# Optimization experiments

Hardware: AMD Instinct MI355X
Metric: run time of the kernel (lower is better)

Reference implementation:

```python
import jax, jax.numpy as jnp
import numpy as np

SELF_LOOP_EPS = 0.5

def setup_inputs() -> dict:
    key = jax.random.key(0)
    k1, k2 = jax.random.split(key)
    spatial_nodes = jax.random.normal(k1, (16, 2048, 64), dtype=jnp.float32)
    temporal_nodes = jax.random.normal(k2, (16, 64, 64), dtype=jnp.float32)
    return {"spatial_nodes": spatial_nodes, "temporal_nodes": temporal_nodes}

def reference(spatial_nodes, temporal_nodes):
    # concat spatial and temporal node embeddings along the node axis: [B, N+T, D]
    node_embs = jnp.concatenate([spatial_nodes, temporal_nodes], axis=1)
    # batched gram matrix: [B, M, M], M = N+T
    adj = jnp.einsum('bnf,bmf->bnm', node_embs, node_embs)
    adj = jnp.tanh(jax.nn.relu(adj))
    M = adj.shape[1]
    # add scaled self loops
    adj = adj + jnp.eye(M, dtype=adj.dtype) * SELF_LOOP_EPS
    # the torch module additionally extracts per-batch nonzero (edge_index, edge_weight)
    # lists; that is data-dependent stream compaction. The dense adj (plus its nonzero
    # mask) carries the identical information in a jit-compatible fixed-shape form.
    return adj
```

## Files before the change

### kernel.cpp

```cpp
#include <hip/hip_runtime.h>
#include <hip/hip_fp16.h>


#define B_BATCH   16
#define N_SPATIAL 2048
#define T_TEMP    64
#define M_NODES   2112
#define D_FEAT    64
#define TILE      64
#define LDSK      72
#define CSTR      68

#define TILES_PER_BATCH 1089
#define TOTAL_TILES     17424
#define TILES_PER_XCD   2178

typedef _Float16 f16x8 __attribute__((ext_vector_type(8)));
typedef float    f32x4 __attribute__((ext_vector_type(4)));

__global__ __launch_bounds__(256, 4)
void gram_tanh_mfma(const float* __restrict__ sp,
                    const float* __restrict__ tp,
                    float* __restrict__ out)
{
    const int lin = blockIdx.x;
    const int t   = (lin & 7) * TILES_PER_XCD + (lin >> 3);
    const int b   = t / TILES_PER_BATCH;
    const int r   = t - b * TILES_PER_BATCH;
    const int ti  = r / 33;
    const int tj  = r - ti * 33;

    __shared__ __align__(16) _Float16 As[TILE][LDSK];
    __shared__ __align__(16) _Float16 Bs[TILE][LDSK];
    __shared__ __align__(16) float    Ct[TILE][CSTR];

    const int tid = threadIdx.x;

    {
        const int row = tid >> 2;
        const int kb  = (tid & 3) * 16;
        const float* srcA = (ti < 32)
            ? sp + ((size_t)b * N_SPATIAL + (size_t)ti * TILE) * D_FEAT
            : tp + (size_t)b * T_TEMP * D_FEAT;
        const float* srcB = (tj < 32)
            ? sp + ((size_t)b * N_SPATIAL + (size_t)tj * TILE) * D_FEAT
            : tp + (size_t)b * T_TEMP * D_FEAT;
        const float4* pa = (const float4*)(srcA + (size_t)row * D_FEAT + kb);
        const float4* pb = (const float4*)(srcB + (size_t)row * D_FEAT + kb);

        f16x8 ha0, ha1, hb0, hb1;
        #pragma unroll
        for (int u = 0; u < 2; ++u) {
            float4 a = pa[u];
            ha0[u*4+0] = (_Float16)a.x; ha0[u*4+1] = (_Float16)a.y;
            ha0[u*4+2] = (_Float16)a.z; ha0[u*4+3] = (_Float16)a.w;
            float4 bb = pb[u];
            hb0[u*4+0] = (_Float16)bb.x; hb0[u*4+1] = (_Float16)bb.y;
            hb0[u*4+2] = (_Float16)bb.z; hb0[u*4+3] = (_Float16)bb.w;
        }
        #pragma unroll
        for (int u = 0; u < 2; ++u) {
            float4 a = pa[2+u];
            ha1[u*4+0] = (_Float16)a.x; ha1[u*4+1] = (_Float16)a.y;
            ha1[u*4+2] = (_Float16)a.z; ha1[u*4+3] = (_Float16)a.w;
            float4 bb = pb[2+u];
            hb1[u*4+0] = (_Float16)bb.x; hb1[u*4+1] = (_Float16)bb.y;
            hb1[u*4+2] = (_Float16)bb.z; hb1[u*4+3] = (_Float16)bb.w;
        }
        *(f16x8*)&As[row][kb]     = ha0;
        *(f16x8*)&As[row][kb + 8] = ha1;
        *(f16x8*)&Bs[row][kb]     = hb0;
        *(f16x8*)&Bs[row][kb + 8] = hb1;
    }
    __syncthreads();

    const int wave = tid >> 6;
    const int lane = tid & 63;
    const int lr   = lane & 15;
    const int q    = lane >> 4;

    f32x4 acc[4];
    #pragma unroll
    for (int tt = 0; tt < 4; ++tt) acc[tt] = (f32x4){0.f, 0.f, 0.f, 0.f};

    #pragma unroll
    for (int s = 0; s < 2; ++s) {
        f16x8 afrag = *(const f16x8*)&As[wave * 16 + lr][s * 32 + q * 8];
        #pragma unroll
        for (int tt = 0; tt < 4; ++tt) {
            f16x8 bfrag = *(const f16x8*)&Bs[tt * 16 + lr][s * 32 + q * 8];
            acc[tt] = __builtin_amdgcn_mfma_f32_16x16x32_f16(afrag, bfrag, acc[tt], 0, 0, 0);
        }
    }

    const bool diagTile = (ti == tj);
    #pragma unroll
    for (int tt = 0; tt < 4; ++tt) {
        const int col = tt * 16 + lr;
        #pragma unroll
        for (int i = 0; i < 4; ++i) {
            const int row = wave * 16 + q * 4 + i;
            float x = fmaxf(acc[tt][i], 0.f);
            float e = __expf(2.f * x);
            float v = 1.f - 2.f * __builtin_amdgcn_rcpf(e + 1.f);
            if (diagTile && (row == col)) v += 0.5f;
            Ct[row][col] = v;
        }
    }
    __syncthreads();

    {
        const int row = tid >> 2;
        float* dst = out + (size_t)b * M_NODES * M_NODES
                         + (size_t)(ti * TILE + row) * M_NODES + tj * TILE;
        #pragma unroll
        for (int u = 0; u < 4; ++u) {
            const int c4 = (tid & 3) * 4 + 16 * u;
            *(float4*)(dst + c4) = *(const float4*)&Ct[row][c4];
        }
    }
}

extern "C" void kernel_launch(void* const* d_in, const int* in_sizes, int n_in,
                              void* d_out, int out_size, void* d_ws, size_t ws_size,
                              hipStream_t stream) {
    const float* sp = (const float*)d_in[0];
    const float* tp = (const float*)d_in[1];
    float* out = (float*)d_out;

    dim3 grid(TOTAL_TILES);
    dim3 block(256);
    hipLaunchKernelGGL(gram_tanh_mfma, grid, block, 0, stream, sp, tp, out);
}
```

Baseline: 281.3 us.

## Compute two column tiles per workgroup and drop the block barrier before stores

Each workgroup now loads one A row-strip and two adjacent B column tiles, then computes two 64x64 output tiles. This halves the grid size and reuses the A-tile load and conversion across both. The epilogue has each wave write its own 16 rows straight from LDS, which removes the second __syncthreads. The XCD mapping now gives two whole batches to each XCD. The cost is more LDS and registers per workgroup, with the launch-bounds occupancy hint lowered from 4 to 3.

Result: no change. 279.5 us (-0.6%).

```diff
diff --git a/kernel.cpp b/kernel.cpp
--- a/kernel.cpp
+++ b/kernel.cpp
@@ -11,27 +11,43 @@
 #define LDSK      72
 #define CSTR      68
 
-#define TILES_PER_BATCH 1089
-#define TOTAL_TILES     17424
-#define TILES_PER_XCD   2178
+#define GROUPS_PER_STRIP 17
+#define WGS_PER_BATCH    (33 * GROUPS_PER_STRIP)
+#define TOTAL_WGS        (WGS_PER_BATCH * B_BATCH)
+#define WGS_PER_XCD      (TOTAL_WGS / 8)
 
 typedef _Float16 f16x8 __attribute__((ext_vector_type(8)));
 typedef float    f32x4 __attribute__((ext_vector_type(4)));
 
-__global__ __launch_bounds__(256, 4)
+__device__ __forceinline__ f16x8 cvt2(const float4* p) {
+    float4 a = p[0], c = p[1];
+    f16x8 h;
+    h[0] = (_Float16)a.x; h[1] = (_Float16)a.y;
+    h[2] = (_Float16)a.z; h[3] = (_Float16)a.w;
+    h[4] = (_Float16)c.x; h[5] = (_Float16)c.y;
+    h[6] = (_Float16)c.z; h[7] = (_Float16)c.w;
+    return h;
+}
+
+__global__ __launch_bounds__(256, 3)
 void gram_tanh_mfma(const float* __restrict__ sp,
                     const float* __restrict__ tp,
                     float* __restrict__ out)
 {
     const int lin = blockIdx.x;
-    const int t   = (lin & 7) * TILES_PER_XCD + (lin >> 3);
-    const int b   = t / TILES_PER_BATCH;
-    const int r   = t - b * TILES_PER_BATCH;
-    const int ti  = r / 33;
-    const int tj  = r - ti * 33;
+    const int xcd = lin & 7;
+    const int l   = lin >> 3;
+    const int bo  = l / WGS_PER_BATCH;
+    const int rr  = l - bo * WGS_PER_BATCH;
+    const int ti  = rr / GROUPS_PER_STRIP;
+    const int g   = rr - ti * GROUPS_PER_STRIP;
+    const int b   = 2 * xcd + bo;
+    const int tj0 = 2 * g;
+    const bool have2 = (tj0 + 1 < 33);
+    const int tj1 = have2 ? tj0 + 1 : 32;
 
     __shared__ __align__(16) _Float16 As[TILE][LDSK];
-    __shared__ __align__(16) _Float16 Bs[TILE][LDSK];
+    __shared__ __align__(16) _Float16 Bs[2][TILE][LDSK];
     __shared__ __align__(16) float    Ct[TILE][CSTR];
 
     const int tid = threadIdx.x;
@@ -42,35 +58,22 @@
         const float* srcA = (ti < 32)
             ? sp + ((size_t)b * N_SPATIAL + (size_t)ti * TILE) * D_FEAT
             : tp + (size_t)b * T_TEMP * D_FEAT;
-        const float* srcB = (tj < 32)
-            ? sp + ((size_t)b * N_SPATIAL + (size_t)tj * TILE) * D_FEAT
+        const float* srcB0 = (tj0 < 32)
+            ? sp + ((size_t)b * N_SPATIAL + (size_t)tj0 * TILE) * D_FEAT
             : tp + (size_t)b * T_TEMP * D_FEAT;
-        const float4* pa = (const float4*)(srcA + (size_t)row * D_FEAT + kb);
-        const float4* pb = (const float4*)(srcB + (size_t)row * D_FEAT + kb);
+        const float* srcB1 = (tj1 < 32)
+            ? sp + ((size_t)b * N_SPATIAL + (size_t)tj1 * TILE) * D_FEAT
+            : tp + (size_t)b * T_TEMP * D_FEAT;
+        const float4* pa  = (const float4*)(srcA  + (size_t)row * D_FEAT + kb);
+        const float4* pb0 = (const float4*)(srcB0 + (size_t)row * D_FEAT + kb);
+        const float4* pb1 = (const float4*)(srcB1 + (size_t)row * D_FEAT + kb);
 
-        f16x8 ha0, ha1, hb0, hb1;
-        #pragma unroll
-        for (int u = 0; u < 2; ++u) {
-            float4 a = pa[u];
-            ha0[u*4+0] = (_Float16)a.x; ha0[u*4+1] = (_Float16)a.y;
-            ha0[u*4+2] = (_Float16)a.z; ha0[u*4+3] = (_Float16)a.w;
-            float4 bb = pb[u];
-            hb0[u*4+0] = (_Float16)bb.x; hb0[u*4+1] = (_Float16)bb.y;
-            hb0[u*4+2] = (_Float16)bb.z; hb0[u*4+3] = (_Float16)bb.w;
-        }
-        #pragma unroll
-        for (int u = 0; u < 2; ++u) {
-            float4 a = pa[2+u];
-            ha1[u*4+0] = (_Float16)a.x; ha1[u*4+1] = (_Float16)a.y;
-            ha1[u*4+2] = (_Float16)a.z; ha1[u*4+3] = (_Float16)a.w;
-            float4 bb = pb[2+u];
-            hb1[u*4+0] = (_Float16)bb.x; hb1[u*4+1] = (_Float16)bb.y;
-            hb1[u*4+2] = (_Float16)bb.z; hb1[u*4+3] = (_Float16)bb.w;
-        }
-        *(f16x8*)&As[row][kb]     = ha0;
-        *(f16x8*)&As[row][kb + 8] = ha1;
-        *(f16x8*)&Bs[row][kb]     = hb0;
-        *(f16x8*)&Bs[row][kb + 8] = hb1;
+        *(f16x8*)&As[row][kb]        = cvt2(pa);
+        *(f16x8*)&As[row][kb + 8]    = cvt2(pa + 2);
+        *(f16x8*)&Bs[0][row][kb]     = cvt2(pb0);
+        *(f16x8*)&Bs[0][row][kb + 8] = cvt2(pb0 + 2);
+        *(f16x8*)&Bs[1][row][kb]     = cvt2(pb1);
+        *(f16x8*)&Bs[1][row][kb + 8] = cvt2(pb1 + 2);
     }
     __syncthreads();
 
@@ -79,44 +82,51 @@
     const int lr   = lane & 15;
     const int q    = lane >> 4;
 
-    f32x4 acc[4];
+    f32x4 acc[2][4];
     #pragma unroll
-    for (int tt = 0; tt < 4; ++tt) acc[tt] = (f32x4){0.f, 0.f, 0.f, 0.f};
+    for (int n = 0; n < 2; ++n)
+        #pragma unroll
+        for (int tt = 0; tt < 4; ++tt) acc[n][tt] = (f32x4){0.f, 0.f, 0.f, 0.f};
 
     #pragma unroll
     for (int s = 0; s < 2; ++s) {
         f16x8 afrag = *(const f16x8*)&As[wave * 16 + lr][s * 32 + q * 8];
         #pragma unroll
-        for (int tt = 0; tt < 4; ++tt) {
-            f16x8 bfrag = *(const f16x8*)&Bs[tt * 16 + lr][s * 32 + q * 8];
-            acc[tt] = __builtin_amdgcn_mfma_f32_16x16x32_f16(afrag, bfrag, acc[tt], 0, 0, 0);
+        for (int n = 0; n < 2; ++n) {
+            #pragma unroll
+            for (int tt = 0; tt < 4; ++tt) {
+                f16x8 bfrag = *(const f16x8*)&Bs[n][tt * 16 + lr][s * 32 + q * 8];
+                acc[n][tt] = __builtin_amdgcn_mfma_f32_16x16x32_f16(afrag, bfrag, acc[n][tt], 0, 0, 0);
+            }
         }
     }
 
-    const bool diagTile = (ti == tj);
     #pragma unroll
-    for (int tt = 0; tt < 4; ++tt) {
-        const int col = tt * 16 + lr;
+    for (int n = 0; n < 2; ++n) {
+        if (n == 1 && !have2) break;
+        const int tjn = n ? tj1 : tj0;
+        const bool diagT = (ti == tjn);
         #pragma unroll
-        for (int i = 0; i < 4; ++i) {
-            const int row = wave * 16 + q * 4 + i;
-            float x = fmaxf(acc[tt][i], 0.f);
-            float e = __expf(2.f * x);
-            float v = 1.f - 2.f * __builtin_amdgcn_rcpf(e + 1.f);
-            if (diagTile && (row == col)) v += 0.5f;
-            Ct[row][col] = v;
+        for (int tt = 0; tt < 4; ++tt) {
+            const int col = tt * 16 + lr;
+            #pragma unroll
+            for (int i = 0; i < 4; ++i) {
+                const int row = wave * 16 + q * 4 + i;
+                float x = fmaxf(acc[n][tt][i], 0.f);
+                float e = __expf(2.f * x);
+                float v = 1.f - 2.f * __builtin_amdgcn_rcpf(e + 1.f);
+                if (diagT && (row == col)) v += 0.5f;
+                Ct[row][col] = v;
+            }
         }
-    }
-    __syncthreads();
-
-    {
-        const int row = tid >> 2;
+        const int rs = lane >> 2;
         float* dst = out + (size_t)b * M_NODES * M_NODES
-                         + (size_t)(ti * TILE + row) * M_NODES + tj * TILE;
+                         + (size_t)(ti * TILE + wave * 16 + rs) * M_NODES
+                         + tjn * TILE;
         #pragma unroll
         for (int u = 0; u < 4; ++u) {
-            const int c4 = (tid & 3) * 4 + 16 * u;
-            *(float4*)(dst + c4) = *(const float4*)&Ct[row][c4];
+            const int c4 = (lane & 3) * 4 + 16 * u;
+            *(float4*)(dst + c4) = *(const float4*)&Ct[wave * 16 + rs][c4];
         }
     }
 }
@@ -128,7 +138,7 @@
     const float* tp = (const float*)d_in[1];
     float* out = (float*)d_out;
 
-    dim3 grid(TOTAL_TILES);
+    dim3 grid(TOTAL_WGS);
     dim3 block(256);
     hipLaunchKernelGGL(gram_tanh_mfma, grid, block, 0, stream, sp, tp, out);
 }
```
